# Kernel tuning notes

Hardware: AMD Instinct MI355X
Metric: run time of the kernel (lower is better)

Reference implementation:

```python
import jax, jax.numpy as jnp
import numpy as np

B, N, H, D = 4, 2048, 4, 32
ALL = H * D          # all_key_dim == all_value_dim == 128
OUT = 128            # output_dim
QC, KC = 512, 512    # q_chunk_size, kv_chunk_size
NEG_INF = -1e30


def setup_inputs() -> dict:
    key = jax.random.key(0)
    ks = jax.random.split(key, 9)
    s = 1.0 / np.sqrt(ALL).astype(np.float32)
    return {
        "q_data": jax.random.normal(ks[0], (B, N, ALL), jnp.float32),
        "m_data": jax.random.normal(ks[1], (B, N, ALL), jnp.float32),
        "bias": 0.1 * jax.random.normal(ks[2], (B, N, N), jnp.float32),
        "nonbatched_bias": 0.1 * jax.random.normal(ks[3], (H, N, N), jnp.float32),
        "Wq": s * jax.random.normal(ks[4], (ALL, ALL), jnp.float32),
        "Wk": s * jax.random.normal(ks[5], (ALL, ALL), jnp.float32),
        "Wv": s * jax.random.normal(ks[6], (ALL, ALL), jnp.float32),
        "Wg": s * jax.random.normal(ks[7], (ALL, ALL), jnp.float32),
        "bg": jnp.zeros((ALL,), jnp.float32),
        "Wo": s * jax.random.normal(ks[8], (ALL, OUT), jnp.float32),
        "bo": jnp.zeros((OUT,), jnp.float32),
    }


def _flash_attention(q, k, v, bias, nb_bias, qc, kc):
    """Chunked online-softmax attention (iterative_qkv).
    q,k,v: [B,N,H,D]; bias: [B,Q,K]; nb_bias: [H,Q,K]. Returns [B,Q,H,D]."""
    Bq, Q, Hn, Dd = q.shape
    K = k.shape[1]
    nq, nk = Q // qc, K // kc
    # q chunks leading: [nq, B, qc, H, D]
    q_ch = q.reshape(Bq, nq, qc, Hn, Dd).transpose(1, 0, 2, 3, 4)
    # kv chunks leading (scanned): [nk, B, kc, H, D]
    k_ch = k.reshape(Bq, nk, kc, Hn, Dd).transpose(1, 0, 2, 3, 4)
    v_ch = v.reshape(Bq, nk, kc, Hn, Dd).transpose(1, 0, 2, 3, 4)
    # biases: [nq, nk, B, qc, kc] and [nq, nk, H, qc, kc]
    b_ch = bias.reshape(Bq, nq, qc, nk, kc).transpose(1, 3, 0, 2, 4)
    nb_ch = nb_bias.reshape(Hn, nq, qc, nk, kc).transpose(1, 3, 0, 2, 4)

    def one_q_chunk(q_c, b_qc, nb_qc):
        def kv_step(carry, xs):
            m, l, acc = carry
            k_c, v_c, bb, nn = xs
            # scores: [B,H,qc,kc]
            s = jnp.einsum('bqhd,bkhd->bhqk', q_c, k_c)
            s = s + bb[:, None, :, :] + nn[None, :, :, :]
            m_new = jnp.maximum(m, jax.lax.stop_gradient(s).max(axis=-1))
            alpha = jnp.exp(m - m_new)
            p = jnp.exp(s - m_new[..., None])
            l_new = l * alpha + p.sum(axis=-1)
            acc_new = acc * alpha[..., None] + jnp.einsum('bhqk,bkhd->bhqd', p, v_c)
            return (m_new, l_new, acc_new), None

        m0 = jnp.full((Bq, Hn, qc), NEG_INF, q.dtype)
        l0 = jnp.zeros((Bq, Hn, qc), q.dtype)
        a0 = jnp.zeros((Bq, Hn, qc, Dd), q.dtype)
        (m, l, acc), _ = jax.lax.scan(kv_step, (m0, l0, a0), (k_ch, v_ch, b_qc, nb_qc))
        return (acc / l[..., None]).transpose(0, 2, 1, 3)  # [B,qc,H,D]

    out = jax.vmap(one_q_chunk)(q_ch, b_ch, nb_ch)  # [nq,B,qc,H,D]
    return out.transpose(1, 0, 2, 3, 4).reshape(Bq, Q, Hn, Dd)


def reference(q_data, m_data, bias, nonbatched_bias, Wq, Wk, Wv, Wg, bg, Wo, bo):
    Bq, Nq, ad = q_data.shape
    h = nonbatched_bias.shape[0]
    d = ad // h
    q = (q_data @ Wq).reshape(Bq, Nq, h, d)
    k = (m_data @ Wk).reshape(Bq, Nq, h, d)
    v = (m_data @ Wv).reshape(Bq, Nq, h, d)
    wa = _flash_attention(q, k, v, bias, nonbatched_bias, QC, KC)
    gate = jax.nn.sigmoid(q_data @ Wg + bg).reshape(Bq, Nq, h, d)
    wa = wa * gate
    return wa.reshape(Bq, Nq, ad) @ Wo + bo
```

## Files before the change

kernel.cpp:

```cpp
#include <hip/hip_runtime.h>
#include <cstdint>
#include <cstddef>

typedef __bf16 bf16x8 __attribute__((ext_vector_type(8)));
typedef unsigned short u16x8 __attribute__((ext_vector_type(8)));
typedef float f32x4 __attribute__((ext_vector_type(4)));
typedef unsigned u32x4 __attribute__((ext_vector_type(4)));

#define MFMA(a, b, c) __builtin_amdgcn_mfma_f32_16x16x32_bf16(a, b, c, 0, 0, 0)
#define WAITV(N) asm volatile("s_waitcnt vmcnt(" #N ")" ::: "memory")
#define SBAR()   __builtin_amdgcn_sched_barrier(0)

__device__ __forceinline__ unsigned short f2bfbits(float x) {
    unsigned u = __builtin_bit_cast(unsigned, x);
    u += 0x7FFFu + ((u >> 16) & 1u);
    return (unsigned short)(u >> 16);
}

__device__ __forceinline__ unsigned cvt_pk(float lo, float hi) {
    unsigned r;
    asm("v_cvt_pk_bf16_f32 %0, %1, %2" : "=v"(r) : "v"(lo), "v"(hi));
    return r;
}

__device__ __forceinline__ bf16x8 pack8(f32x4 a, f32x4 b) {
    u32x4 t = { cvt_pk(a[0], a[1]), cvt_pk(a[2], a[3]),
                cvt_pk(b[0], b[1]), cvt_pk(b[2], b[3]) };
    return __builtin_bit_cast(bf16x8, t);
}

__device__ __forceinline__ void gl_lds16(const void* g, void* l) {
    __builtin_amdgcn_global_load_lds(
        (const __attribute__((address_space(1))) unsigned int*)g,
        (__attribute__((address_space(3))) unsigned int*)l, 16, 0, 0);
}

__global__ __launch_bounds__(256) void proj_kernel(
    const float* __restrict__ q_data, const float* __restrict__ m_data,
    const float* __restrict__ Wq, const float* __restrict__ Wk,
    const float* __restrict__ Wv, const float* __restrict__ Wg,
    const float* __restrict__ bg,
    unsigned short* __restrict__ Qb, unsigned short* __restrict__ Kb,
    unsigned short* __restrict__ VT, float* __restrict__ gate)
{
    __shared__ unsigned short vt_lds[128][80];
    const int mat   = blockIdx.x >> 7;
    const int mtile = blockIdx.x & 127;
    const int wave  = threadIdx.x >> 6;
    const int lane  = threadIdx.x & 63;
    const int r16 = lane & 15, g = lane >> 4;
    const int rowbase = mtile * 64 + wave * 16;

    const float* src = (mat == 1 || mat == 2) ? m_data : q_data;
    const float* W   = (mat == 0) ? Wq : (mat == 1) ? Wk : (mat == 2) ? Wv : Wg;

    bf16x8 afrag[4];
    {
        const float* arow = src + (size_t)(rowbase + r16) * 128;
        #pragma unroll
        for (int kk = 0; kk < 4; ++kk) {
            f32x4 lo = *(const f32x4*)(arow + kk * 32 + g * 8);
            f32x4 hi = *(const f32x4*)(arow + kk * 32 + g * 8 + 4);
            afrag[kk] = pack8(lo, hi);
        }
    }

    f32x4 acc[8];
    #pragma unroll
    for (int n0 = 0; n0 < 8; ++n0) {
        f32x4 a = {0.f, 0.f, 0.f, 0.f};
        #pragma unroll
        for (int kk = 0; kk < 4; ++kk) {
            f32x4 lo, hi;
            #pragma unroll
            for (int i = 0; i < 4; ++i) {
                lo[i] = W[(size_t)(kk * 32 + g * 8 + i) * 128 + n0 * 16 + r16];
                hi[i] = W[(size_t)(kk * 32 + g * 8 + 4 + i) * 128 + n0 * 16 + r16];
            }
            a = MFMA(afrag[kk], pack8(lo, hi), a);
        }
        acc[n0] = a;
    }

    if (mat <= 1) {
        unsigned short* dst = (mat == 0) ? Qb : Kb;
        #pragma unroll
        for (int n0 = 0; n0 < 8; ++n0) {
            int n = n0 * 16 + r16, h = n >> 5, d = n & 31;
            #pragma unroll
            for (int i = 0; i < 4; ++i) {
                int grow = rowbase + 4 * g + i;
                int bb = grow >> 11, ns = grow & 2047;
                dst[(size_t)(bb * 4 + h) * 65536 + (size_t)ns * 32 + d] =
                    f2bfbits(acc[n0][i]);
            }
        }
    } else if (mat == 2) {
        #pragma unroll
        for (int n0 = 0; n0 < 8; ++n0) {
            int n = n0 * 16 + r16;
            #pragma unroll
            for (int i = 0; i < 4; ++i)
                vt_lds[n][wave * 16 + 4 * g + i] = f2bfbits(acc[n0][i]);
        }
        __syncthreads();
        int bb = rowbase >> 11;
        int nsbase = (mtile * 64) & 2047;
        #pragma unroll
        for (int it = 0; it < 4; ++it) {
            int idx = (threadIdx.x + it * 256) * 8;
            int n = idx >> 6, mm = idx & 63;
            u16x8 v = *(const u16x8*)&vt_lds[n][mm];
            *(u16x8*)(VT + (size_t)(bb * 128 + n) * 2048 + nsbase + mm) = v;
        }
    } else {
        #pragma unroll
        for (int n0 = 0; n0 < 8; ++n0) {
            int n = n0 * 16 + r16;
            float bgv = bg[n];
            #pragma unroll
            for (int i = 0; i < 4; ++i) {
                int grow = rowbase + 4 * g + i;
                float x = acc[n0][i] + bgv;
                gate[(size_t)grow * 128 + n] = 1.0f / (1.0f + __expf(-x));
            }
        }
    }
}

#define NB_OFF 16384
#define K_OFF  49152
#define V_OFF  81920

__global__ __launch_bounds__(512, 2) void attn_kernel(
    const unsigned short* __restrict__ Qb, const unsigned short* __restrict__ Kb,
    const unsigned short* __restrict__ VT,
    const float* __restrict__ bias, const float* __restrict__ nbias,
    float* __restrict__ Pm, float* __restrict__ Pl, float* __restrict__ Pacc)
{
    extern __shared__ __align__(16) char pool[];

    const int split = blockIdx.x >> 7;
    const int rem   = blockIdx.x & 127;
    const int bpair = rem >> 6;
    const int qt32  = rem & 63;
    const int qb32  = qt32 * 32;
    const int kv0   = split * 512;

    const int w    = threadIdx.x >> 6;
    const int h    = w & 3;
    const int qh   = w >> 2;
    const int lane = threadIdx.x & 63;
    const int q16 = lane & 15, g = lane >> 4;

    const int ls8 = lane >> 3, lc8 = lane & 7;
    const int rho = lane >> 2, l4 = lane & 3;
    const int krow_l = ((rho >> 2) << 3) + (rho & 3);

    const float* bias_bq = bias + ((size_t)((bpair * 2 + qh) * 2048 + qb32)) * 2048;
    const float* nb_h    = nbias + ((size_t)(h * 2048 + qb32)) * 2048;
    const unsigned short* Kp_own = Kb + (size_t)((bpair * 2 + qh) * 4 + h) * 65536;
    const unsigned short* Vp_own = VT + (size_t)((bpair * 2 + qh) * 4 + h) * 65536;

    bf16x8 qf0 = *(const bf16x8*)(Qb + (size_t)((bpair * 2 + 0) * 4 + h) * 65536
                                  + (size_t)(qb32 + qh * 16 + q16) * 32 + g * 8);
    bf16x8 qf1 = *(const bf16x8*)(Qb + (size_t)((bpair * 2 + 1) * 4 + h) * 65536
                                  + (size_t)(qb32 + qh * 16 + q16) * 32 + g * 8);

    float m0v = -1e30f, l0v = 0.f, m1v = -1e30f, l1v = 0.f;
    f32x4 a00 = {0, 0, 0, 0}, a01 = {0, 0, 0, 0};
    f32x4 a10 = {0, 0, 0, 0}, a11 = {0, 0, 0, 0};

    auto stage = [&](int it) {
        if (it >= 16) return;
        const int bf = it & 1;
        const int kb = kv0 + it * 32;
        const int csw0 = (lc8 * 4) ^ (ls8 << 2);
        gl_lds16(bias_bq + (size_t)(8 * h + ls8) * 2048 + kb + csw0,
                 pool + bf * 8192 + qh * 4096 + h * 1024);
        #pragma unroll
        for (int c = 0; c < 2; ++c)
            gl_lds16(nb_h + (size_t)(qh * 16 + 8 * c + ls8) * 2048 + kb + csw0,
                     pool + NB_OFF + bf * 16384 + h * 4096 + qh * 2048 + c * 1024);
        #pragma unroll
        for (int t = 0; t < 2; ++t)
            gl_lds16(Kp_own + (size_t)(kb + 4 * t + krow_l) * 32 + l4 * 8,
                     pool + K_OFF + bf * 16384 + qh * 8192 + h * 2048 + t * 1024);
        #pragma unroll
        for (int j = 0; j < 2; ++j)
            gl_lds16(Vp_own + (size_t)(16 * j + rho) * 2048 + kb + l4 * 8,
                     pool + V_OFF + bf * 16384 + qh * 8192 + h * 2048 + j * 1024);
    };

    auto chain = [&](f32x4 s0, f32x4 s1, bf16x8 vf0, bf16x8 vf1,
                     float& m, float& lsum, f32x4& ac0, f32x4& ac1) {
        float mx = fmaxf(fmaxf(fmaxf(s0[0], s0[1]), fmaxf(s0[2], s0[3])),
                         fmaxf(fmaxf(s1[0], s1[1]), fmaxf(s1[2], s1[3])));
        mx = fmaxf(mx, __shfl_xor(mx, 16));
        mx = fmaxf(mx, __shfl_xor(mx, 32));
        float m_new = fmaxf(m, mx);
        float alpha = __expf(m - m_new);
        float ps = 0.f;
        #pragma unroll
        for (int i = 0; i < 4; ++i) { s0[i] = __expf(s0[i] - m_new); ps += s0[i]; }
        #pragma unroll
        for (int i = 0; i < 4; ++i) { s1[i] = __expf(s1[i] - m_new); ps += s1[i]; }
        ps += __shfl_xor(ps, 16);
        ps += __shfl_xor(ps, 32);
        lsum = lsum * alpha + ps;
        m = m_new;
        u32x4 pc = { cvt_pk(s0[0], s0[1]), cvt_pk(s0[2], s0[3]),
                     cvt_pk(s1[0], s1[1]), cvt_pk(s1[2], s1[3]) };
        bf16x8 p = __builtin_bit_cast(bf16x8, pc);
        ac0 *= alpha;
        ac1 *= alpha;
        ac0 = MFMA(vf0, p, ac0);
        ac1 = MFMA(vf1, p, ac1);
    };

    stage(0);

    #pragma unroll 2
    for (int it = 0; it < 16; ++it) {
        const int bf = it & 1;
        if (it < 15) {
            stage(it + 1);
            WAITV(7);
        } else {
            WAITV(0);
        }
        SBAR();
        __builtin_amdgcn_s_barrier();

        const int r128 = (qh * 16 + q16) * 128;
        const int rsw  = (q16 & 7) << 4;
        const char* np = pool + NB_OFF + bf * 16384 + h * 4096;
        f32x4 nn0 = *(const f32x4*)(np + r128 + ((g * 32) ^ rsw));
        f32x4 nn1 = *(const f32x4*)(np + r128 + ((16 + g * 32) ^ rsw));
        const char* bp0 = pool + bf * 8192;
        f32x4 b00 = *(const f32x4*)(bp0 + r128 + ((g * 32) ^ rsw));
        f32x4 b01 = *(const f32x4*)(bp0 + r128 + ((16 + g * 32) ^ rsw));
        const char* bp1 = bp0 + 4096;
        f32x4 b10 = *(const f32x4*)(bp1 + r128 + ((g * 32) ^ rsw));
        f32x4 b11 = *(const f32x4*)(bp1 + r128 + ((16 + g * 32) ^ rsw));
        const char* kp0 = pool + K_OFF + bf * 16384 + h * 2048;
        bf16x8 kf00 = *(const bf16x8*)(kp0 + q16 * 64 + g * 16);
        bf16x8 kf01 = *(const bf16x8*)(kp0 + 1024 + q16 * 64 + g * 16);
        const char* kp1 = kp0 + 8192;
        bf16x8 kf10 = *(const bf16x8*)(kp1 + q16 * 64 + g * 16);
        bf16x8 kf11 = *(const bf16x8*)(kp1 + 1024 + q16 * 64 + g * 16);
        const char* vp0 = pool + V_OFF + bf * 16384 + h * 2048;
        bf16x8 vf00 = *(const bf16x8*)(vp0 + q16 * 64 + g * 16);
        bf16x8 vf01 = *(const bf16x8*)(vp0 + 1024 + q16 * 64 + g * 16);
        const char* vp1 = vp0 + 8192;
        bf16x8 vf10 = *(const bf16x8*)(vp1 + q16 * 64 + g * 16);
        bf16x8 vf11 = *(const bf16x8*)(vp1 + 1024 + q16 * 64 + g * 16);
        asm volatile("s_waitcnt lgkmcnt(0)" ::: "memory");
        SBAR();
        __builtin_amdgcn_s_barrier();

        f32x4 z = {0, 0, 0, 0};
        f32x4 s00 = MFMA(kf00, qf0, z);
        f32x4 s01 = MFMA(kf01, qf0, z);
        s00 += b00 + nn0;
        s01 += b01 + nn1;
        f32x4 s10 = MFMA(kf10, qf1, z);
        f32x4 s11 = MFMA(kf11, qf1, z);
        s10 += b10 + nn0;
        s11 += b11 + nn1;
        chain(s00, s01, vf00, vf01, m0v, l0v, a00, a01);
        chain(s10, s11, vf10, vf11, m1v, l1v, a10, a11);
    }

    {
        const size_t q = (size_t)(qb32 + qh * 16 + q16);
        const size_t p0 = ((size_t)split * 16 + (bpair * 2 + 0) * 4 + h) * 2048 + q;
        const size_t p1 = ((size_t)split * 16 + (bpair * 2 + 1) * 4 + h) * 2048 + q;
        if (g == 0) { Pm[p0] = m0v; Pl[p0] = l0v; Pm[p1] = m1v; Pl[p1] = l1v; }
        float* pa0 = Pacc + p0 * 32;
        float* pa1 = Pacc + p1 * 32;
        #pragma unroll
        for (int i = 0; i < 4; ++i) {
            pa0[4 * g + i]      = a00[i];
            pa0[16 + 4 * g + i] = a01[i];
            pa1[4 * g + i]      = a10[i];
            pa1[16 + 4 * g + i] = a11[i];
        }
    }
}

__global__ __launch_bounds__(256) void combine_kernel(
    const float* __restrict__ Pm, const float* __restrict__ Pl,
    const float* __restrict__ Pacc, const float* __restrict__ gate,
    const float* __restrict__ Wo, const float* __restrict__ bo,
    float* __restrict__ out)
{
    __shared__ unsigned short wa_lds[16][136];

    const int b  = blockIdx.x >> 7;
    const int qb = (blockIdx.x & 127) * 16;
    const int h    = threadIdx.x >> 6;
    const int lane = threadIdx.x & 63;
    const int q16 = lane & 15, g = lane >> 4;
    const size_t bh = (size_t)(b * 4 + h);
    const size_t q  = (size_t)(qb + q16);

    float ms[4], ls[4];
    #pragma unroll
    for (int s = 0; s < 4; ++s) {
        size_t idx = ((size_t)s * 16 + bh) * 2048 + q;
        ms[s] = Pm[idx];
        ls[s] = Pl[idx];
    }
    float M = fmaxf(fmaxf(ms[0], ms[1]), fmaxf(ms[2], ms[3]));
    float e[4];
    float L = 0.f;
    #pragma unroll
    for (int s = 0; s < 4; ++s) { e[s] = __expf(ms[s] - M); L += ls[s] * e[s]; }

    f32x4 o0 = {0, 0, 0, 0}, o1 = {0, 0, 0, 0};
    #pragma unroll
    for (int s = 0; s < 4; ++s) {
        const float* pa = Pacc + (((size_t)s * 16 + bh) * 2048 + q) * 32;
        f32x4 a0 = *(const f32x4*)(pa + 4 * g);
        f32x4 a1 = *(const f32x4*)(pa + 16 + 4 * g);
        o0 += a0 * e[s];
        o1 += a1 * e[s];
    }
    float invL = 1.0f / L;
    const float* grow = gate + ((size_t)b * 2048 + q) * 128 + h * 32;
    f32x4 g0 = *(const f32x4*)(grow + 4 * g);
    f32x4 g1 = *(const f32x4*)(grow + 16 + 4 * g);

    {
        uint2 t0, t1;
        t0.x = cvt_pk(o0[0] * invL * g0[0], o0[1] * invL * g0[1]);
        t0.y = cvt_pk(o0[2] * invL * g0[2], o0[3] * invL * g0[3]);
        t1.x = cvt_pk(o1[0] * invL * g1[0], o1[1] * invL * g1[1]);
        t1.y = cvt_pk(o1[2] * invL * g1[2], o1[3] * invL * g1[3]);
        *(uint2*)&wa_lds[q16][h * 32 + 4 * g]      = t0;
        *(uint2*)&wa_lds[q16][h * 32 + 16 + 4 * g] = t1;
    }
    __syncthreads();

    f32x4 oo0 = {0, 0, 0, 0}, oo1 = {0, 0, 0, 0};
    #pragma unroll
    for (int kk = 0; kk < 4; ++kk) {
        bf16x8 a = *(const bf16x8*)&wa_lds[q16][kk * 32 + g * 8];
        f32x4 l0, h0, l1, h1;
        #pragma unroll
        for (int i = 0; i < 4; ++i) {
            int k0 = kk * 32 + g * 8 + i;
            int k1 = k0 + 4;
            l0[i] = Wo[(size_t)k0 * 128 + h * 32 + q16];
            h0[i] = Wo[(size_t)k1 * 128 + h * 32 + q16];
            l1[i] = Wo[(size_t)k0 * 128 + h * 32 + 16 + q16];
            h1[i] = Wo[(size_t)k1 * 128 + h * 32 + 16 + q16];
        }
        oo0 = MFMA(a, pack8(l0, h0), oo0);
        oo1 = MFMA(a, pack8(l1, h1), oo1);
    }
    float bo0 = bo[h * 32 + q16], bo1 = bo[h * 32 + 16 + q16];
    #pragma unroll
    for (int i = 0; i < 4; ++i) {
        int row = qb + 4 * g + i;
        out[((size_t)b * 2048 + row) * 128 + h * 32 + q16]      = oo0[i] + bo0;
        out[((size_t)b * 2048 + row) * 128 + h * 32 + 16 + q16] = oo1[i] + bo1;
    }
}

extern "C" void kernel_launch(void* const* d_in, const int* in_sizes, int n_in,
                              void* d_out, int out_size, void* d_ws, size_t ws_size,
                              hipStream_t stream)
{
    const float* q_data = (const float*)d_in[0];
    const float* m_data = (const float*)d_in[1];
    const float* bias   = (const float*)d_in[2];
    const float* nbias  = (const float*)d_in[3];
    const float* Wq     = (const float*)d_in[4];
    const float* Wk     = (const float*)d_in[5];
    const float* Wv     = (const float*)d_in[6];
    const float* Wg     = (const float*)d_in[7];
    const float* bg     = (const float*)d_in[8];
    const float* Wo     = (const float*)d_in[9];
    const float* bo     = (const float*)d_in[10];
    float* out = (float*)d_out;

    char* ws = (char*)d_ws;
    unsigned short* Qb = (unsigned short*)(ws);
    unsigned short* Kb = (unsigned short*)(ws + (2u << 20));
    unsigned short* VT = (unsigned short*)(ws + (4u << 20));
    float*          gate = (float*)(ws + (6u << 20));
    float*          Pm = (float*)(ws + (12u << 20));
    float*          Pl = (float*)(ws + (12u << 20) + (512u << 10));
    float*          Pacc = (float*)(ws + (13u << 20));

    proj_kernel<<<dim3(512), dim3(256), 0, stream>>>(
        q_data, m_data, Wq, Wk, Wv, Wg, bg, Qb, Kb, VT, gate);
    attn_kernel<<<dim3(512), dim3(512), 114688, stream>>>(
        Qb, Kb, VT, bias, nbias, Pm, Pl, Pacc);
    combine_kernel<<<dim3(512), dim3(256), 0, stream>>>(
        Pm, Pl, Pacc, gate, Wo, bo, out);
}
```

Measured before the change: 81.86 us.

## Enlarge attention blocks to 64 query rows with 1024 threads sharing K/V tiles

```diff
diff --git a/kernel.cpp b/kernel.cpp
--- a/kernel.cpp
+++ b/kernel.cpp
@@ -130,9 +130,10 @@
 
 #define NB_OFF 16384
 #define K_OFF  49152
-#define V_OFF  81920
-
-__global__ __launch_bounds__(512, 2) void attn_kernel(
+#define V_OFF  65536
+#define SLOT_SZ 81920
+
+__global__ __launch_bounds__(1024, 1) void attn_kernel(
     const unsigned short* __restrict__ Qb, const unsigned short* __restrict__ Kb,
     const unsigned short* __restrict__ VT,
     const float* __restrict__ bias, const float* __restrict__ nbias,
@@ -140,11 +141,11 @@
 {
     extern __shared__ __align__(16) char pool[];
 
-    const int split = blockIdx.x >> 7;
-    const int rem   = blockIdx.x & 127;
-    const int bpair = rem >> 6;
-    const int qt32  = rem & 63;
-    const int qb32  = qt32 * 32;
+    const int split = blockIdx.x >> 6;
+    const int rem   = blockIdx.x & 63;
+    const int bpair = rem >> 5;
+    const int qt    = rem & 31;
+    const int qb64  = qt * 64;
     const int kv0   = split * 512;
 
     const int w    = threadIdx.x >> 6;
@@ -157,15 +158,20 @@
     const int rho = lane >> 2, l4 = lane & 3;
     const int krow_l = ((rho >> 2) << 3) + (rho & 3);
 
-    const float* bias_bq = bias + ((size_t)((bpair * 2 + qh) * 2048 + qb32)) * 2048;
-    const float* nb_h    = nbias + ((size_t)(h * 2048 + qb32)) * 2048;
-    const unsigned short* Kp_own = Kb + (size_t)((bpair * 2 + qh) * 4 + h) * 65536;
-    const unsigned short* Vp_own = VT + (size_t)((bpair * 2 + qh) * 4 + h) * 65536;
-
-    bf16x8 qf0 = *(const bf16x8*)(Qb + (size_t)((bpair * 2 + 0) * 4 + h) * 65536
-                                  + (size_t)(qb32 + qh * 16 + q16) * 32 + g * 8);
-    bf16x8 qf1 = *(const bf16x8*)(Qb + (size_t)((bpair * 2 + 1) * 4 + h) * 65536
-                                  + (size_t)(qb32 + qh * 16 + q16) * 32 + g * 8);
+    const int b0 = bpair * 2, b1 = b0 + 1;
+    const int bsl = qh & 1;
+    const int tsl = qh >> 1;
+
+    const float* bias_w = bias
+        + ((size_t)((b0 + (w >> 3)) * 2048 + qb64 + (w & 7) * 8)) * 2048;
+    const float* nb_w = nbias + ((size_t)(h * 2048 + qb64 + qh * 16)) * 2048;
+    const unsigned short* Kp_w = Kb + (size_t)((b0 + bsl) * 4 + h) * 65536;
+    const unsigned short* Vp_w = VT + (size_t)((b0 + bsl) * 4 + h) * 65536;
+
+    bf16x8 qf0 = *(const bf16x8*)(Qb + (size_t)(b0 * 4 + h) * 65536
+                                  + (size_t)(qb64 + qh * 16 + q16) * 32 + g * 8);
+    bf16x8 qf1 = *(const bf16x8*)(Qb + (size_t)(b1 * 4 + h) * 65536
+                                  + (size_t)(qb64 + qh * 16 + q16) * 32 + g * 8);
 
     float m0v = -1e30f, l0v = 0.f, m1v = -1e30f, l1v = 0.f;
     f32x4 a00 = {0, 0, 0, 0}, a01 = {0, 0, 0, 0};
@@ -175,21 +181,18 @@
         if (it >= 16) return;
         const int bf = it & 1;
         const int kb = kv0 + it * 32;
+        char* base = pool + bf * SLOT_SZ;
         const int csw0 = (lc8 * 4) ^ (ls8 << 2);
-        gl_lds16(bias_bq + (size_t)(8 * h + ls8) * 2048 + kb + csw0,
-                 pool + bf * 8192 + qh * 4096 + h * 1024);
+        gl_lds16(bias_w + (size_t)ls8 * 2048 + kb + csw0,
+                 base + (w >> 3) * 8192 + (w & 7) * 1024);
         #pragma unroll
         for (int c = 0; c < 2; ++c)
-            gl_lds16(nb_h + (size_t)(qh * 16 + 8 * c + ls8) * 2048 + kb + csw0,
-                     pool + NB_OFF + bf * 16384 + h * 4096 + qh * 2048 + c * 1024);
-        #pragma unroll
-        for (int t = 0; t < 2; ++t)
-            gl_lds16(Kp_own + (size_t)(kb + 4 * t + krow_l) * 32 + l4 * 8,
-                     pool + K_OFF + bf * 16384 + qh * 8192 + h * 2048 + t * 1024);
-        #pragma unroll
-        for (int j = 0; j < 2; ++j)
-            gl_lds16(Vp_own + (size_t)(16 * j + rho) * 2048 + kb + l4 * 8,
-                     pool + V_OFF + bf * 16384 + qh * 8192 + h * 2048 + j * 1024);
+            gl_lds16(nb_w + (size_t)(8 * c + ls8) * 2048 + kb + csw0,
+                     base + NB_OFF + h * 8192 + qh * 2048 + c * 1024);
+        gl_lds16(Kp_w + (size_t)(kb + 4 * tsl + krow_l) * 32 + l4 * 8,
+                 base + K_OFF + bsl * 8192 + h * 2048 + tsl * 1024);
+        gl_lds16(Vp_w + (size_t)(16 * tsl + rho) * 2048 + kb + l4 * 8,
+                 base + V_OFF + bsl * 8192 + h * 2048 + tsl * 1024);
     };
 
     auto chain = [&](f32x4 s0, f32x4 s1, bf16x8 vf0, bf16x8 vf1,
@@ -225,31 +228,32 @@
         const int bf = it & 1;
         if (it < 15) {
             stage(it + 1);
-            WAITV(7);
+            WAITV(5);
         } else {
             WAITV(0);
         }
         SBAR();
         __builtin_amdgcn_s_barrier();
 
+        const char* slot = pool + bf * SLOT_SZ;
         const int r128 = (qh * 16 + q16) * 128;
         const int rsw  = (q16 & 7) << 4;
-        const char* np = pool + NB_OFF + bf * 16384 + h * 4096;
+        const char* np = slot + NB_OFF + h * 8192;
         f32x4 nn0 = *(const f32x4*)(np + r128 + ((g * 32) ^ rsw));
         f32x4 nn1 = *(const f32x4*)(np + r128 + ((16 + g * 32) ^ rsw));
-        const char* bp0 = pool + bf * 8192;
+        const char* bp0 = slot;
         f32x4 b00 = *(const f32x4*)(bp0 + r128 + ((g * 32) ^ rsw));
         f32x4 b01 = *(const f32x4*)(bp0 + r128 + ((16 + g * 32) ^ rsw));
-        const char* bp1 = bp0 + 4096;
+        const char* bp1 = bp0 + 8192;
         f32x4 b10 = *(const f32x4*)(bp1 + r128 + ((g * 32) ^ rsw));
         f32x4 b11 = *(const f32x4*)(bp1 + r128 + ((16 + g * 32) ^ rsw));
-        const char* kp0 = pool + K_OFF + bf * 16384 + h * 2048;
+        const char* kp0 = slot + K_OFF + h * 2048;
         bf16x8 kf00 = *(const bf16x8*)(kp0 + q16 * 64 + g * 16);
         bf16x8 kf01 = *(const bf16x8*)(kp0 + 1024 + q16 * 64 + g * 16);
         const char* kp1 = kp0 + 8192;
         bf16x8 kf10 = *(const bf16x8*)(kp1 + q16 * 64 + g * 16);
         bf16x8 kf11 = *(const bf16x8*)(kp1 + 1024 + q16 * 64 + g * 16);
-        const char* vp0 = pool + V_OFF + bf * 16384 + h * 2048;
+        const char* vp0 = slot + V_OFF + h * 2048;
         bf16x8 vf00 = *(const bf16x8*)(vp0 + q16 * 64 + g * 16);
         bf16x8 vf01 = *(const bf16x8*)(vp0 + 1024 + q16 * 64 + g * 16);
         const char* vp1 = vp0 + 8192;
@@ -273,9 +277,9 @@
     }
 
     {
-        const size_t q = (size_t)(qb32 + qh * 16 + q16);
-        const size_t p0 = ((size_t)split * 16 + (bpair * 2 + 0) * 4 + h) * 2048 + q;
-        const size_t p1 = ((size_t)split * 16 + (bpair * 2 + 1) * 4 + h) * 2048 + q;
+        const size_t q = (size_t)(qb64 + qh * 16 + q16);
+        const size_t p0 = ((size_t)split * 16 + (b0 * 4 + h)) * 2048 + q;
+        const size_t p1 = ((size_t)split * 16 + (b1 * 4 + h)) * 2048 + q;
         if (g == 0) { Pm[p0] = m0v; Pl[p0] = l0v; Pm[p1] = m1v; Pl[p1] = l1v; }
         float* pa0 = Pacc + p0 * 32;
         float* pa1 = Pacc + p1 * 32;
@@ -397,7 +401,7 @@
 
     proj_kernel<<<dim3(512), dim3(256), 0, stream>>>(
         q_data, m_data, Wq, Wk, Wv, Wg, bg, Qb, Kb, VT, gate);
-    attn_kernel<<<dim3(512), dim3(512), 114688, stream>>>(
+    attn_kernel<<<dim3(256), dim3(1024), 163840, stream>>>(
         Qb, Kb, VT, bias, nbias, Pm, Pl, Pacc);
     combine_kernel<<<dim3(512), dim3(256), 0, stream>>>(
         Pm, Pl, Pacc, gate, Wo, bo, out);
```

Result: faster. 68.08 us (-16.8%).
